# Kernel optimization log

Hardware: AMD Instinct MI355X
Metric: run time of the kernel (lower is better)

## Reference

```python
import jax, jax.numpy as jnp
import numpy as np

BATCH = 4096
M = 50        # CEM candidates per state
N_TOP = 32    # elites
ITERS = 100   # sequential CEM iterations
HIDDEN = 100


def setup_inputs() -> dict:
    key = jax.random.key(0)
    ks = jax.random.split(key, 7)
    states = jax.random.normal(ks[0], (BATCH, 2), dtype=jnp.float32)
    W1 = jax.random.normal(ks[1], (3, HIDDEN), dtype=jnp.float32) * 0.1
    b1 = jnp.zeros((HIDDEN,), dtype=jnp.float32)
    W2 = jax.random.normal(ks[2], (HIDDEN, HIDDEN), dtype=jnp.float32) * 0.1
    b2 = jnp.zeros((HIDDEN,), dtype=jnp.float32)
    W3 = jax.random.normal(ks[3], (HIDDEN, 1), dtype=jnp.float32) * 0.1
    b3 = jnp.zeros((1,), dtype=jnp.float32)
    return {"states": states, "W1": W1, "b1": b1, "W2": W2, "b2": b2, "W3": W3, "b3": b3}


def reference(states, W1, b1, W2, b2, W3, b3):
    batch = states.shape[0]
    states_bm = jnp.broadcast_to(states[:, None, :], (batch, M, 2))

    def qnet(angles):  # angles: (batch, M) -> q: (batch, M)
        x = jnp.concatenate([states_bm, angles[..., None]], axis=-1)  # (batch, M, 3)
        h = jax.nn.relu(x @ W1 + b1)
        h = jax.nn.relu(h @ W2 + b2)
        return (h @ W3 + b3)[..., 0]

    key = jax.random.key(42)
    k0, kloop = jax.random.split(key)
    # iteration 0: uniform random angles in [0, 1)
    angles0 = jax.random.uniform(k0, (batch, M), dtype=jnp.float32)
    q0 = qnet(angles0)

    def step(q, k):
        # NOTE: faithful to source — elites/mu/std are over Q-VALUES, and
        # new "angles" are sampled from Normal(mu_q, std_q).
        top = jax.lax.top_k(q, N_TOP)[0]                 # (batch, N_TOP)
        mu = top.mean(-1)                                # (batch,)
        std = top.std(-1, ddof=1)                        # torch unbiased std
        eps = jax.random.normal(k, (batch, M), dtype=jnp.float32)
        angles = mu[:, None] + std[:, None] * eps        # reparameterized normal
        return qnet(angles), mu

    keys = jax.random.split(kloop, ITERS - 1)
    _, mus = jax.lax.scan(step, q0, keys)
    return mus[-1] * (2.0 * jnp.pi)
```

## Files before the change

kernel.cpp:

```cpp
#include <hip/hip_runtime.h>
#include <math.h>
#include <stdint.h>

#define BATCH 4096
#define MCAND 50
#define NTOP 32
#define HID 100
#define EPS_ROWS 98
#define EPS_ROWSZ (BATCH*MCAND)
#define EPS_ELEMS (EPS_ROWS*EPS_ROWSZ)
#define WS_NEED   (1024u + (size_t)EPS_ELEMS*4u)

#define MINVC  (-0x1.fffffep-1f)
#define SQRT2C (0x1.6a09e6p+0f)

__device__ __forceinline__ uint32_t rotl32(uint32_t v, int d){ return (v<<d)|(v>>(32-d)); }

__device__ __forceinline__ void tf2x32(uint32_t k0, uint32_t k1, uint32_t x0, uint32_t x1,
                                       uint32_t &o0, uint32_t &o1){
  uint32_t k2 = k0 ^ k1 ^ 0x1BD11BDAu;
  x0 += k0; x1 += k1;
#define RND(r) { x0 += x1; x1 = rotl32(x1,(r)); x1 ^= x0; }
  RND(13) RND(15) RND(26) RND(6)
  x0 += k1; x1 += k2 + 1u;
  RND(17) RND(29) RND(16) RND(24)
  x0 += k2; x1 += k0 + 2u;
  RND(13) RND(15) RND(26) RND(6)
  x0 += k0; x1 += k1 + 3u;
  RND(17) RND(29) RND(16) RND(24)
  x0 += k1; x1 += k2 + 4u;
  RND(13) RND(15) RND(26) RND(6)
  x0 += k2; x1 += k0 + 5u;
#undef RND
  o0 = x0; o1 = x1;
}

__device__ __forceinline__ float erfinv32(float x){
  float w = -log1pf(-x*x);
  float p;
  if (w < 5.0f){
    w = w - 2.5f;
    p = 2.81022636e-08f;
    p = fmaf(p, w, 3.43273939e-07f);
    p = fmaf(p, w, -3.5233877e-06f);
    p = fmaf(p, w, -4.39150654e-06f);
    p = fmaf(p, w, 0.00021858087f);
    p = fmaf(p, w, -0.00125372503f);
    p = fmaf(p, w, -0.00417768164f);
    p = fmaf(p, w, 0.246640727f);
    p = fmaf(p, w, 1.50140941f);
  } else {
    w = sqrtf(w) - 3.0f;
    p = -0.000200214257f;
    p = fmaf(p, w, 0.000100950558f);
    p = fmaf(p, w, 0.00134934322f);
    p = fmaf(p, w, -0.00367342844f);
    p = fmaf(p, w, 0.00573950773f);
    p = fmaf(p, w, -0.0076224613f);
    p = fmaf(p, w, 0.00943887047f);
    p = fmaf(p, w, 1.00167406f);
    p = fmaf(p, w, 2.83297682f);
  }
  return p*x;
}

#define DPPF(v, CTRL) __int_as_float(__builtin_amdgcn_update_dpp( \
    0, __float_as_int(v), (CTRL), 0xF, 0xF, true))
#define DPPI(v, CTRL) __builtin_amdgcn_update_dpp(0, (v), (CTRL), 0xF, 0xF, true)
#define DPPADD(v, CTRL) ((v) + DPPF((v), (CTRL)))

__device__ __forceinline__ float fswap4(float v){
  float a = DPPF(v, 0x114);
  float b = DPPF(v, 0x104);
  return (threadIdx.x & 4) ? a : b;
}
__device__ __forceinline__ int iswap4(int v){
  int a = DPPI(v, 0x114), b = DPPI(v, 0x104);
  return (threadIdx.x & 4) ? a : b;
}
__device__ __forceinline__ float fswap8(float v){
  return DPPF(v, 0x128);
}
__device__ __forceinline__ float fswap16(float v){
#if __has_builtin(__builtin_amdgcn_permlane16_swap)
  auto r = __builtin_amdgcn_permlane16_swap(__float_as_uint(v), __float_as_uint(v), false, false);
  return __uint_as_float((threadIdx.x & 16) ? r[0] : r[1]);
#else
  return __shfl_xor(v, 16, 64);
#endif
}
__device__ __forceinline__ float fswap32(float v){
#if __has_builtin(__builtin_amdgcn_permlane32_swap)
  auto r = __builtin_amdgcn_permlane32_swap(__float_as_uint(v), __float_as_uint(v), false, false);
  return __uint_as_float((threadIdx.x & 32) ? r[0] : r[1]);
#else
  return __shfl_xor(v, 32, 64);
#endif
}

__global__ void keys_kernel(uint32_t* __restrict__ K){
  int tid = threadIdx.x;
  if (tid < 99){
    uint32_t A0, B0, A1, B1;
    tf2x32(0u,42u,0u,2u,A0,A1);
    tf2x32(0u,42u,1u,3u,B0,B1);
    (void)A0; (void)B0;
    uint32_t o0,o1;
    tf2x32(A1,B1,(uint32_t)tid,(uint32_t)(99+tid),o0,o1);
    K[tid]    = o0;
    K[99+tid] = o1;
  }
}

__global__ __launch_bounds__(256) void eps_kernel(const uint32_t* __restrict__ K,
                                                  float* __restrict__ E){
  int id = blockIdx.x*256 + threadIdx.x;
  int t  = id / EPS_ROWSZ;
  int g  = id - t*EPS_ROWSZ;
  uint32_t kk0 = K[2*t], kk1 = K[2*t+1];
  uint32_t r0, r1, bits;
  if ((uint32_t)g < 102400u){ tf2x32(kk0,kk1,(uint32_t)g,(uint32_t)g+102400u,r0,r1); bits = r0; }
  else                      { tf2x32(kk0,kk1,(uint32_t)g-102400u,(uint32_t)g,r0,r1); bits = r1; }
  float fl = __uint_as_float((bits>>9) | 0x3f800000u) - 1.0f;
  float u  = fmaxf(MINVC, fl*2.0f + MINVC);
  E[id] = SQRT2C * erfinv32(u);
}

template<bool EPSG>
__global__ __launch_bounds__(512, 4) void cem_kernel(
    const float* __restrict__ states, const float* __restrict__ W1,
    const float* __restrict__ b1,     const float* __restrict__ W2,
    const float* __restrict__ b2,     const float* __restrict__ W3,
    const float* __restrict__ b3,     const float* __restrict__ epsg,
    float* __restrict__ out)
{
  __shared__ __align__(16) float smem[20400];
  float2* const T2D  = (float2*)smem;
  int*    const ORD  = (int*)(smem + 300);
  float*  const ST   = smem + 400;
  float*  const A    = smem + 20200;
  float*  const QB   = smem + 20250;
  float*  const EPB  = smem + 20300;

  const int tid  = threadIdx.x;
  const int b    = blockIdx.x;
  const int wv   = tid >> 6;
  const int lane = tid & 63;
  const int gc   = tid >> 3;
  const int gj   = tid & 7;
  const bool gact = (tid < 8*MCAND);

  float w3r[13];
#pragma unroll
  for (int i = 0; i < 13; ++i){
    int n = gj + (i<<3);
    w3r[i] = (n < HID) ? W3[n] : 0.0f;
  }
  const float sB3v = b3[0];

  if (tid < HID){
    float u = fmaf(states[2*b], W1[tid], fmaf(states[2*b+1], W1[HID+tid], b1[tid]));
    float v = W1[2*HID+tid];
    float tt = (v != 0.0f) ? (-u / v) : INFINITY;
    smem[tid]     = u;
    smem[HID+tid] = v;
    smem[200+tid] = tt;
  }
  __syncthreads();

  if (tid < HID){
    float tk = smem[200+tid];
    int rk = 0;
    for (int j2 = 0; j2 < HID; ++j2){
      float tj = smem[200+j2];
      rk += (tj < tk || (tj == tk && j2 < tid)) ? 1 : 0;
    }
    float u = smem[tid], v = smem[HID+tid];
    int neg = (v < 0.0f || (v == 0.0f && u > 0.0f)) ? 1 : 0;
    ST[rk]  = tk;
    ORD[rk] = tid | (neg << 7);
  }
  __syncthreads();

  int kpA = 0, kpB = 0; float cuA = 0.f, cvA = 0.f, cuB = 0.f, cvB = 0.f;
  if (wv == 0){
    kpA = ORD[lane];
    int kiA = kpA & 127;
    float uA = smem[kiA], vA = smem[HID+kiA];
    cuA = (kpA & 128) ? -uA : uA;
    cvA = (kpA & 128) ? -vA : vA;
    if (lane < 36){
      kpB = ORD[64+lane];
      int kiB = kpB & 127;
      float uB = smem[kiB], vB = smem[HID+kiB];
      cuB = (kpB & 128) ? -uB : uB;
      cvB = (kpB & 128) ? -vB : vB;
    }
  }
  float st_r[13];
#pragma unroll
  for (int i = 0; i < 13; ++i){
    int idx = gj*13 + i;
    st_r[i] = (idx < HID) ? ST[idx] : INFINITY;
  }
  __syncthreads();

  uint32_t A1k = 0u, B1k = 0u;
  if (wv == 0){
    const int L = lane;
    float a10 = b2[L], a20 = 0.0f;
    float a11 = (L < 36) ? b2[64+L] : 0.0f, a21 = 0.0f;
#pragma unroll 8
    for (int rr = 0; rr < 64; ++rr){
      int   kp = __builtin_amdgcn_readlane(kpA, rr);
      float cu = __int_as_float(__builtin_amdgcn_readlane(__float_as_int(cuA), rr));
      float cv = __int_as_float(__builtin_amdgcn_readlane(__float_as_int(cvA), rr));
      int k = kp & 127;
      float bu = (kp & 128) ? -cu : 0.0f;
      float bv = (kp & 128) ? -cv : 0.0f;
      float w0 = W2[k*HID + L];
      a10 = fmaf(bu, w0, a10); a20 = fmaf(bv, w0, a20);
      if (L < 36){
        float w1 = W2[k*HID + 64+L];
        a11 = fmaf(bu, w1, a11); a21 = fmaf(bv, w1, a21);
      }
    }
#pragma unroll 6
    for (int rr = 0; rr < 36; ++rr){
      int   kp = __builtin_amdgcn_readlane(kpB, rr);
      float cu = __int_as_float(__builtin_amdgcn_readlane(__float_as_int(cuB), rr));
      float cv = __int_as_float(__builtin_amdgcn_readlane(__float_as_int(cvB), rr));
      int k = kp & 127;
      float bu = (kp & 128) ? -cu : 0.0f;
      float bv = (kp & 128) ? -cv : 0.0f;
      float w0 = W2[k*HID + L];
      a10 = fmaf(bu, w0, a10); a20 = fmaf(bv, w0, a20);
      if (L < 36){
        float w1 = W2[k*HID + 64+L];
        a11 = fmaf(bu, w1, a11); a21 = fmaf(bv, w1, a21);
      }
    }
    { float2 f; f.x = a10; f.y = a20; T2D[L] = f; }
    if (L < 36){ float2 f; f.x = a11; f.y = a21; T2D[64+L] = f; }
#pragma unroll 8
    for (int rr = 0; rr < 64; ++rr){
      int   kp = __builtin_amdgcn_readlane(kpA, rr);
      float cu = __int_as_float(__builtin_amdgcn_readlane(__float_as_int(cuA), rr));
      float cv = __int_as_float(__builtin_amdgcn_readlane(__float_as_int(cvA), rr));
      int k = kp & 127;
      float w0 = W2[k*HID + L];
      a10 = fmaf(cu, w0, a10); a20 = fmaf(cv, w0, a20);
      { float2 f; f.x = a10; f.y = a20; T2D[(rr+1)*HID + L] = f; }
      if (L < 36){
        float w1 = W2[k*HID + 64+L];
        a11 = fmaf(cu, w1, a11); a21 = fmaf(cv, w1, a21);
        float2 f; f.x = a11; f.y = a21; T2D[(rr+1)*HID + 64+L] = f;
      }
    }
#pragma unroll 6
    for (int rr = 0; rr < 36; ++rr){
      int   kp = __builtin_amdgcn_readlane(kpB, rr);
      float cu = __int_as_float(__builtin_amdgcn_readlane(__float_as_int(cuB), rr));
      float cv = __int_as_float(__builtin_amdgcn_readlane(__float_as_int(cvB), rr));
      int k = kp & 127;
      float w0 = W2[k*HID + L];
      a10 = fmaf(cu, w0, a10); a20 = fmaf(cv, w0, a20);
      { float2 f; f.x = a10; f.y = a20; T2D[(65+rr)*HID + L] = f; }
      if (L < 36){
        float w1 = W2[k*HID + 64+L];
        a11 = fmaf(cu, w1, a11); a21 = fmaf(cv, w1, a21);
        float2 f; f.x = a11; f.y = a21; T2D[(65+rr)*HID + 64+L] = f;
      }
    }
  } else if (wv == 7){
    uint32_t A0, B0, a1t, b1t;
    tf2x32(0u,42u,0u,2u,A0,a1t);
    tf2x32(0u,42u,1u,3u,B0,b1t);
    A1k = a1t; B1k = b1t;
    if (lane < MCAND){
      uint32_t gidx = (uint32_t)b*MCAND + (uint32_t)lane;
      uint32_t r0, r1, bits;
      if (gidx < 102400u){ tf2x32(A0,B0,gidx,gidx+102400u,r0,r1); bits = r0; }
      else               { tf2x32(A0,B0,gidx-102400u,gidx,r0,r1); bits = r1; }
      A[lane] = __uint_as_float((bits>>9) | 0x3f800000u) - 1.0f;
    }
  }
  __syncthreads();

#pragma unroll 1
  for (int t = 0; t < 99; ++t){
    float epsv = 0.0f;
    if (EPSG){
      if (wv == 0 && lane < MCAND && t < EPS_ROWS)
        epsv = epsg[(size_t)t*EPS_ROWSZ + (size_t)b*MCAND + (size_t)lane];
    }
    if (gact){
      const float av = A[gc];
      int rk = 0;
#pragma unroll
      for (int i = 0; i < 13; ++i) rk += (st_r[i] < av) ? 1 : 0;
      rk += DPPI(rk, 0xB1);
      rk += DPPI(rk, 0x4E);
      rk += iswap4(rk);
      const float2* __restrict__ Trow = T2D + rk*HID;
      float acc = 0.0f;
#pragma unroll
      for (int i = 0; i < 13; ++i){
        int n = gj + (i<<3);
        n = (n < HID) ? n : gj;
        float2 tv = Trow[n];
        float h = fmaxf(fmaf(av, tv.y, tv.x), 0.0f);
        acc = fmaf(h, w3r[i], acc);
      }
      acc = DPPADD(acc, 0xB1);
      acc = DPPADD(acc, 0x4E);
      acc += fswap4(acc);
      if (gj == 0) QB[gc] = acc;
    }
    if (!EPSG && wv == 7 && t < EPS_ROWS){
      uint32_t kk0, kk1;
      { uint32_t i0 = 2u*(uint32_t)t; uint32_t ii = (i0 < 99u) ? i0 : (i0 - 99u);
        uint32_t x, y; tf2x32(A1k,B1k, ii, 99u+ii, x, y); kk0 = (i0 < 99u) ? x : y; }
      { uint32_t i1 = 2u*(uint32_t)t + 1u; uint32_t ii = (i1 < 99u) ? i1 : (i1 - 99u);
        uint32_t x, y; tf2x32(A1k,B1k, ii, 99u+ii, x, y); kk1 = (i1 < 99u) ? x : y; }
      if (lane < MCAND){
        uint32_t gidx = (uint32_t)b*MCAND + (uint32_t)lane;
        uint32_t r0, r1, bits;
        if (gidx < 102400u){ tf2x32(kk0,kk1,gidx,gidx+102400u,r0,r1); bits = r0; }
        else               { tf2x32(kk0,kk1,gidx-102400u,gidx,r0,r1); bits = r1; }
        float fl = __uint_as_float((bits>>9) | 0x3f800000u) - 1.0f;
        float u  = fmaxf(MINVC, fl*2.0f + MINVC);
        EPB[lane] = SQRT2C * erfinv32(u);
      }
    }
    __syncthreads();

    if (wv == 0){
      float q = (lane < MCAND) ? (QB[lane] + sB3v) : -INFINITY;
      float v = q;
#define BST(KK, JJ, PV) { float pv = (PV); bool lower = (lane & (JJ)) == 0; \
        bool asc = (lane & (KK)) != 0; float mn = fminf(v, pv), mx = fmaxf(v, pv); \
        v = (lower == asc) ? mn : mx; }
      BST(2, 1,  DPPF(v, 0xB1))
      BST(4, 2,  DPPF(v, 0x4E))
      BST(4, 1,  DPPF(v, 0xB1))
      BST(8, 4,  fswap4(v))
      BST(8, 2,  DPPF(v, 0x4E))
      BST(8, 1,  DPPF(v, 0xB1))
      BST(16, 8, fswap8(v))
      BST(16, 4, fswap4(v))
      BST(16, 2, DPPF(v, 0x4E))
      BST(16, 1, DPPF(v, 0xB1))
      BST(32, 16, fswap16(v))
      BST(32, 8,  fswap8(v))
      BST(32, 4,  fswap4(v))
      BST(32, 2,  DPPF(v, 0x4E))
      BST(32, 1,  DPPF(v, 0xB1))
#undef BST
      {
        float pv = fswap32(v);
        v = ((lane & 32) == 0) ? fmaxf(v, pv) : fminf(v, pv);
      }
      float sv = (lane < NTOP) ? v : 0.0f;
      sv += fswap32(sv);
      sv += fswap16(sv);
      sv += fswap8(sv);
      sv += fswap4(sv);
      sv = DPPADD(sv, 0x4E);
      sv = DPPADD(sv, 0xB1);
      float mun = sv / 32.0f;
      float dv = (lane < NTOP) ? (v - mun) : 0.0f;
      float s2 = dv*dv;
      s2 += fswap32(s2);
      s2 += fswap16(s2);
      s2 += fswap8(s2);
      s2 += fswap4(s2);
      s2 = DPPADD(s2, 0x4E);
      s2 = DPPADD(s2, 0xB1);
      float stdv = sqrtf(s2 / 31.0f);
      if (t == 98){
        if (lane == 0) out[b] = mun * 6.2831854820251465f;
      } else if (lane < MCAND){
        float e = EPSG ? epsv : EPB[lane];
        A[lane] = fmaf(stdv, e, mun);
      }
    }
    __syncthreads();
  }
}

extern "C" void kernel_launch(void* const* d_in, const int* in_sizes, int n_in,
                              void* d_out, int out_size, void* d_ws, size_t ws_size,
                              hipStream_t stream) {
  const float* states = (const float*)d_in[0];
  const float* W1     = (const float*)d_in[1];
  const float* b1     = (const float*)d_in[2];
  const float* W2     = (const float*)d_in[3];
  const float* b2     = (const float*)d_in[4];
  const float* W3     = (const float*)d_in[5];
  const float* b3     = (const float*)d_in[6];
  float* out = (float*)d_out;

  if (d_ws != nullptr && ws_size >= WS_NEED){
    uint32_t* K = (uint32_t*)d_ws;
    float*    E = (float*)((char*)d_ws + 1024);
    hipLaunchKernelGGL(keys_kernel, dim3(1), dim3(128), 0, stream, K);
    hipLaunchKernelGGL(eps_kernel, dim3(EPS_ELEMS/256), dim3(256), 0, stream, K, E);
    hipLaunchKernelGGL(HIP_KERNEL_NAME(cem_kernel<true>), dim3(BATCH), dim3(512), 0, stream,
                       states, W1, b1, W2, b2, W3, b3, (const float*)E, out);
  } else {
    hipLaunchKernelGGL(HIP_KERNEL_NAME(cem_kernel<false>), dim3(BATCH), dim3(512), 0, stream,
                       states, W1, b1, W2, b2, W3, b3, (const float*)nullptr, out);
  }
}
```

Before: 1.315 ms.

## Fuse eps generation into CEM kernel with per-block layout and batched eps loads

Removes the separate keys and eps kernels and has idle waves in each CEM block compute that block's 98x50 normal samples during setup, writing them contiguously in the workspace. The main loop then loads three iterations of eps at a time into shared memory from one wave, replacing a per-iteration strided global load. It also widens the T2D reads to float4, processing two hidden units per load. The costs are longer setup per block, slightly more shared memory, and writes to global memory that must be visible to the block's own later reads.

```diff
diff --git a/kernel.cpp b/kernel.cpp
--- a/kernel.cpp
+++ b/kernel.cpp
@@ -7,9 +7,8 @@
 #define NTOP 32
 #define HID 100
 #define EPS_ROWS 98
-#define EPS_ROWSZ (BATCH*MCAND)
-#define EPS_ELEMS (EPS_ROWS*EPS_ROWSZ)
-#define WS_NEED   (1024u + (size_t)EPS_ELEMS*4u)
+#define EPS_BLK  (EPS_ROWS*MCAND)
+#define WS_NEED  ((size_t)BATCH*EPS_BLK*4u)
 
 #define MINVC  (-0x1.fffffep-1f)
 #define SQRT2C (0x1.6a09e6p+0f)
@@ -98,43 +97,15 @@
 #endif
 }
 
-__global__ void keys_kernel(uint32_t* __restrict__ K){
-  int tid = threadIdx.x;
-  if (tid < 99){
-    uint32_t A0, B0, A1, B1;
-    tf2x32(0u,42u,0u,2u,A0,A1);
-    tf2x32(0u,42u,1u,3u,B0,B1);
-    (void)A0; (void)B0;
-    uint32_t o0,o1;
-    tf2x32(A1,B1,(uint32_t)tid,(uint32_t)(99+tid),o0,o1);
-    K[tid]    = o0;
-    K[99+tid] = o1;
-  }
-}
-
-__global__ __launch_bounds__(256) void eps_kernel(const uint32_t* __restrict__ K,
-                                                  float* __restrict__ E){
-  int id = blockIdx.x*256 + threadIdx.x;
-  int t  = id / EPS_ROWSZ;
-  int g  = id - t*EPS_ROWSZ;
-  uint32_t kk0 = K[2*t], kk1 = K[2*t+1];
-  uint32_t r0, r1, bits;
-  if ((uint32_t)g < 102400u){ tf2x32(kk0,kk1,(uint32_t)g,(uint32_t)g+102400u,r0,r1); bits = r0; }
-  else                      { tf2x32(kk0,kk1,(uint32_t)g-102400u,(uint32_t)g,r0,r1); bits = r1; }
-  float fl = __uint_as_float((bits>>9) | 0x3f800000u) - 1.0f;
-  float u  = fmaxf(MINVC, fl*2.0f + MINVC);
-  E[id] = SQRT2C * erfinv32(u);
-}
-
 template<bool EPSG>
 __global__ __launch_bounds__(512, 4) void cem_kernel(
     const float* __restrict__ states, const float* __restrict__ W1,
     const float* __restrict__ b1,     const float* __restrict__ W2,
     const float* __restrict__ b2,     const float* __restrict__ W3,
-    const float* __restrict__ b3,     const float* __restrict__ epsg,
+    const float* __restrict__ b3,     float* __restrict__ epsg,
     float* __restrict__ out)
 {
-  __shared__ __align__(16) float smem[20400];
+  __shared__ __align__(16) float smem[20452];
   float2* const T2D  = (float2*)smem;
   int*    const ORD  = (int*)(smem + 300);
   float*  const ST   = smem + 400;
@@ -150,11 +121,13 @@
   const int gj   = tid & 7;
   const bool gact = (tid < 8*MCAND);
 
-  float w3r[13];
+  float w3a[7], w3b[7];
 #pragma unroll
-  for (int i = 0; i < 13; ++i){
-    int n = gj + (i<<3);
-    w3r[i] = (n < HID) ? W3[n] : 0.0f;
+  for (int i = 0; i < 7; ++i){
+    int p = gj + (i<<3);
+    bool valid = (p < MCAND);
+    w3a[i] = valid ? W3[2*p]   : 0.0f;
+    w3b[i] = valid ? W3[2*p+1] : 0.0f;
   }
   const float sB3v = b3[0];
 
@@ -272,27 +245,64 @@
         float2 f; f.x = a11; f.y = a21; T2D[(65+rr)*HID + 64+L] = f;
       }
     }
+  } else if (EPSG){
+    uint32_t A0c, B0c, A1c, B1c;
+    tf2x32(0u,42u,0u,2u,A0c,A1c);
+    tf2x32(0u,42u,1u,3u,B0c,B1c);
+    if (wv == 1 && lane < MCAND){
+      uint32_t gidx = (uint32_t)b*MCAND + (uint32_t)lane;
+      uint32_t r0,r1,bits;
+      if (gidx < 102400u){ tf2x32(A0c,B0c,gidx,gidx+102400u,r0,r1); bits = r0; }
+      else               { tf2x32(A0c,B0c,gidx-102400u,gidx,r0,r1); bits = r1; }
+      A[lane] = __uint_as_float((bits>>9) | 0x3f800000u) - 1.0f;
+    }
+    const int idx0 = tid - 64;
+    const int tt   = idx0 >> 2;
+    if (tt < EPS_ROWS){
+      const int c0  = (idx0 & 3) * 13;
+      const int cnt = (c0 == 39) ? 11 : 13;
+      uint32_t kk0, kk1;
+      { uint32_t mi = 2u*(uint32_t)tt;      uint32_t ii = (mi < 99u) ? mi : (mi - 99u);
+        uint32_t x,y; tf2x32(A1c,B1c, ii, 99u+ii, x, y); kk0 = (mi < 99u) ? x : y; }
+      { uint32_t mi = 2u*(uint32_t)tt + 1u; uint32_t ii = (mi < 99u) ? mi : (mi - 99u);
+        uint32_t x,y; tf2x32(A1c,B1c, ii, 99u+ii, x, y); kk1 = (mi < 99u) ? x : y; }
+      float* Eb = epsg + (size_t)b*EPS_BLK + (size_t)tt*MCAND;
+      for (int c = c0; c < c0+cnt; ++c){
+        uint32_t gidx = (uint32_t)b*MCAND + (uint32_t)c;
+        uint32_t r0,r1,bits;
+        if (gidx < 102400u){ tf2x32(kk0,kk1,gidx,gidx+102400u,r0,r1); bits = r0; }
+        else               { tf2x32(kk0,kk1,gidx-102400u,gidx,r0,r1); bits = r1; }
+        float fl = __uint_as_float((bits>>9) | 0x3f800000u) - 1.0f;
+        float u  = fmaxf(MINVC, fl*2.0f + MINVC);
+        Eb[c] = SQRT2C * erfinv32(u);
+      }
+    }
   } else if (wv == 7){
-    uint32_t A0, B0, a1t, b1t;
-    tf2x32(0u,42u,0u,2u,A0,a1t);
-    tf2x32(0u,42u,1u,3u,B0,b1t);
+    uint32_t A0c, B0c, a1t, b1t;
+    tf2x32(0u,42u,0u,2u,A0c,a1t);
+    tf2x32(0u,42u,1u,3u,B0c,b1t);
     A1k = a1t; B1k = b1t;
     if (lane < MCAND){
       uint32_t gidx = (uint32_t)b*MCAND + (uint32_t)lane;
-      uint32_t r0, r1, bits;
-      if (gidx < 102400u){ tf2x32(A0,B0,gidx,gidx+102400u,r0,r1); bits = r0; }
-      else               { tf2x32(A0,B0,gidx-102400u,gidx,r0,r1); bits = r1; }
+      uint32_t r0,r1,bits;
+      if (gidx < 102400u){ tf2x32(A0c,B0c,gidx,gidx+102400u,r0,r1); bits = r0; }
+      else               { tf2x32(A0c,B0c,gidx-102400u,gidx,r0,r1); bits = r1; }
       A[lane] = __uint_as_float((bits>>9) | 0x3f800000u) - 1.0f;
     }
   }
   __syncthreads();
 
+  int tm3 = 0;
 #pragma unroll 1
   for (int t = 0; t < 99; ++t){
-    float epsv = 0.0f;
-    if (EPSG){
-      if (wv == 0 && lane < MCAND && t < EPS_ROWS)
-        epsv = epsg[(size_t)t*EPS_ROWSZ + (size_t)b*MCAND + (size_t)lane];
+    if (EPSG && wv == 7 && tm3 == 0 && t < EPS_ROWS){
+      const float* Eb = epsg + (size_t)b*EPS_BLK + (size_t)t*MCAND;
+      const int lim = EPS_BLK - t*MCAND;
+#pragma unroll
+      for (int j = 0; j < 3; ++j){
+        int idx = j*64 + lane;
+        if (idx < 150 && idx < lim) EPB[idx] = Eb[idx];
+      }
     }
     if (gact){
       const float av = A[gc];
@@ -302,15 +312,17 @@
       rk += DPPI(rk, 0xB1);
       rk += DPPI(rk, 0x4E);
       rk += iswap4(rk);
-      const float2* __restrict__ Trow = T2D + rk*HID;
+      const float4* __restrict__ Trow4 = (const float4*)(T2D + rk*HID);
       float acc = 0.0f;
 #pragma unroll
-      for (int i = 0; i < 13; ++i){
-        int n = gj + (i<<3);
-        n = (n < HID) ? n : gj;
-        float2 tv = Trow[n];
-        float h = fmaxf(fmaf(av, tv.y, tv.x), 0.0f);
-        acc = fmaf(h, w3r[i], acc);
+      for (int i = 0; i < 7; ++i){
+        int p = gj + (i<<3);
+        p = (p < MCAND) ? p : (MCAND-1);
+        float4 tv = Trow4[p];
+        float h0 = fmaxf(fmaf(av, tv.y, tv.x), 0.0f);
+        float h1 = fmaxf(fmaf(av, tv.w, tv.z), 0.0f);
+        acc = fmaf(h0, w3a[i], acc);
+        acc = fmaf(h1, w3b[i], acc);
       }
       acc = DPPADD(acc, 0xB1);
       acc = DPPADD(acc, 0x4E);
@@ -381,11 +393,12 @@
       if (t == 98){
         if (lane == 0) out[b] = mun * 6.2831854820251465f;
       } else if (lane < MCAND){
-        float e = EPSG ? epsv : EPB[lane];
+        float e = EPSG ? EPB[tm3*MCAND + lane] : EPB[lane];
         A[lane] = fmaf(stdv, e, mun);
       }
     }
     __syncthreads();
+    tm3 = (tm3 == 2) ? 0 : tm3 + 1;
   }
 }
 
@@ -402,14 +415,10 @@
   float* out = (float*)d_out;
 
   if (d_ws != nullptr && ws_size >= WS_NEED){
-    uint32_t* K = (uint32_t*)d_ws;
-    float*    E = (float*)((char*)d_ws + 1024);
-    hipLaunchKernelGGL(keys_kernel, dim3(1), dim3(128), 0, stream, K);
-    hipLaunchKernelGGL(eps_kernel, dim3(EPS_ELEMS/256), dim3(256), 0, stream, K, E);
     hipLaunchKernelGGL(HIP_KERNEL_NAME(cem_kernel<true>), dim3(BATCH), dim3(512), 0, stream,
-                       states, W1, b1, W2, b2, W3, b3, (const float*)E, out);
+                       states, W1, b1, W2, b2, W3, b3, (float*)d_ws, out);
   } else {
     hipLaunchKernelGGL(HIP_KERNEL_NAME(cem_kernel<false>), dim3(BATCH), dim3(512), 0, stream,
-                       states, W1, b1, W2, b2, W3, b3, (const float*)nullptr, out);
-  }
-}
+                       states, W1, b1, W2, b2, W3, b3, (float*)nullptr, out);
+  }
+}
```

New measurement: 1.339 ms. About the same (+1.8%).
